# Kernel optimization log

Hardware: AMD Instinct MI355X
Metric: run time of the kernel (lower is better)

Reference implementation:

```python
import jax, jax.numpy as jnp
import numpy as np

DIM = 192
NH = 4
B, H, W = 4, 128, 128


def _conv1x1(x, w, b):
    # x: [b,c,h,w], w: [o,c], b: [o]
    return jnp.einsum('oc,bchw->bohw', w, x) + b[None, :, None, None]


def _dwconv3(x, w, b):
    # depthwise 3x3, w: [C,1,3,3]
    y = jax.lax.conv_general_dilated(
        x, w, window_strides=(1, 1), padding='SAME',
        feature_group_count=x.shape[1],
        dimension_numbers=('NCHW', 'OIHW', 'NCHW'))
    return y + b[None, :, None, None]


def _to_heads(x, nh):
    b, c, h, w = x.shape
    return x.reshape(b, nh, c // nh, h * w)  # b head c (hw)


def _l2norm(x):
    # torch F.normalize(dim=-1): x / max(||x||, eps)
    n = jnp.sqrt(jnp.sum(x * x, axis=-1, keepdims=True))
    return x / jnp.maximum(n, 1e-12)


def _chan_attn(q, k, v, temp):
    # q,k,v: [b,head,c,n]; temp: [head,1,1] -> broadcasts over [b,head,c,c]
    scores = jnp.einsum('bhcn,bhdn->bhcd', q, k) * temp
    a = jax.nn.softmax(scores, axis=-1)
    return jnp.einsum('bhcd,bhdn->bhcn', a, v)


def setup_inputs() -> dict:
    key = jax.random.key(0)
    ks = jax.random.split(key, 16)
    d3 = 3 * DIM
    inp = {
        'sar': jax.random.normal(ks[0], (B, DIM, H, W), jnp.float32),
        'ms': jax.random.normal(ks[1], (B, DIM, H, W), jnp.float32),
        'ms_qkv_w': jax.random.normal(ks[2], (d3, DIM), jnp.float32) * 0.02,
        'ms_qkv_b': jnp.zeros((d3,), jnp.float32),
        'ms_dw_w': jax.random.normal(ks[3], (d3, 1, 3, 3), jnp.float32) * 0.1,
        'ms_dw_b': jnp.zeros((d3,), jnp.float32),
        'ms_temp': jnp.ones((NH, 1, 1), jnp.float32),
        'sar_qkv_w': jax.random.normal(ks[4], (d3, DIM), jnp.float32) * 0.02,
        'sar_qkv_b': jnp.zeros((d3,), jnp.float32),
        'sar_dw_w': jax.random.normal(ks[5], (d3, 1, 3, 3), jnp.float32) * 0.1,
        'sar_dw_b': jnp.zeros((d3,), jnp.float32),
        'sar_temp': jnp.ones((NH, 1, 1), jnp.float32),
        'ms_proj_w': jax.random.normal(ks[6], (DIM, 2 * DIM), jnp.float32) * 0.02,
        'ms_proj_b': jnp.zeros((DIM,), jnp.float32),
        'sar_proj_w': jax.random.normal(ks[7], (DIM, DIM), jnp.float32) * 0.02,
        'sar_proj_b': jnp.zeros((DIM,), jnp.float32),
    }
    return inp


def reference(sar, ms, ms_qkv_w, ms_qkv_b, ms_dw_w, ms_dw_b, ms_temp,
              sar_qkv_w, sar_qkv_b, sar_dw_w, sar_dw_b, sar_temp,
              ms_proj_w, ms_proj_b, sar_proj_w, sar_proj_b):
    b, c, h, w = ms.shape

    ms_qkv = _dwconv3(_conv1x1(ms, ms_qkv_w, ms_qkv_b), ms_dw_w, ms_dw_b)
    ms_q, ms_k, ms_v = jnp.split(ms_qkv, 3, axis=1)
    ms_q = _l2norm(_to_heads(ms_q, NH))
    ms_k = _l2norm(_to_heads(ms_k, NH))
    ms_v = _to_heads(ms_v, NH)

    sar_qkv = _dwconv3(_conv1x1(sar, sar_qkv_w, sar_qkv_b), sar_dw_w, sar_dw_b)
    sar_q, sar_k, sar_v = jnp.split(sar_qkv, 3, axis=1)
    sar_q = _l2norm(_to_heads(sar_q, NH))
    sar_k = _l2norm(_to_heads(sar_k, NH))
    sar_v = _to_heads(sar_v, NH)

    ms_self = _chan_attn(ms_q, ms_k, ms_v, ms_temp).reshape(b, c, h, w)
    sar_self = _chan_attn(sar_q, sar_k, sar_v, sar_temp).reshape(b, c, h, w)
    cross = _chan_attn(sar_q, ms_k, sar_v, ms_temp).reshape(b, c, h, w)

    sar_out = sar + _conv1x1(sar_self, sar_proj_w, sar_proj_b)
    ms_cat = jnp.concatenate([ms_self, cross + ms_self], axis=1)
    ms_out = ms + _conv1x1(ms_cat, ms_proj_w, ms_proj_b)
    return (sar_out, ms_out)
```

## Files before the change

kernel.cpp:

```cpp
#include <hip/hip_runtime.h>
#include <hip/hip_bf16.h>
#include <cstdint>

#define DIMC 192
#define BB 4
#define NN 16384
#define D3 576
#define CHD 48
#define WWID 128
#define HHGT 128
#define NCK 64
#define CKW 256

typedef short short8 __attribute__((ext_vector_type(8)));
typedef float f32x4 __attribute__((ext_vector_type(4)));

union FragU { uint4 u4; short8 s8; };

__device__ __forceinline__ float bf2f(uint16_t v) {
    return __uint_as_float(((uint32_t)v) << 16);
}
__device__ __forceinline__ float2 upk2(uint32_t u) {
    float2 r;
    r.x = __uint_as_float(u << 16);
    r.y = __uint_as_float(u & 0xffff0000u);
    return r;
}
__device__ __forceinline__ uint16_t f2bf(float f) {
    uint32_t x = __float_as_uint(f);
    return (uint16_t)((x + 0x7fffu + ((x >> 16) & 1u)) >> 16);
}
__device__ __forceinline__ uint4 pack8(const uint16_t* v) {
    uint4 u;
    u.x = (uint32_t)v[0] | ((uint32_t)v[1] << 16);
    u.y = (uint32_t)v[2] | ((uint32_t)v[3] << 16);
    u.z = (uint32_t)v[4] | ((uint32_t)v[5] << 16);
    u.w = (uint32_t)v[6] | ((uint32_t)v[7] << 16);
    return u;
}
__device__ __forceinline__ uint4 packf8(float4 lo, float4 hi) {
    uint16_t vv[8] = {f2bf(lo.x), f2bf(lo.y), f2bf(lo.z), f2bf(lo.w),
                      f2bf(hi.x), f2bf(hi.y), f2bf(hi.z), f2bf(hi.w)};
    return pack8(vv);
}

__global__ __launch_bounds__(256, 2) void k_conv_both(
    const float* __restrict__ ms, const float* __restrict__ sarp,
    const float* __restrict__ w_ms, const float* __restrict__ w_sar,
    const float* __restrict__ b_ms, const float* __restrict__ b_sar,
    uint16_t* __restrict__ out_ms, uint16_t* __restrict__ out_sar)
{
    __shared__ uint16_t xs[128][200];
    __shared__ uint16_t wst[64][200];
    const int t = threadIdx.x;
    const int bid = blockIdx.x;
    const int path = bid >> 9;
    const int rem = bid & 511;
    const int nb = rem & 127;
    const int b = rem >> 7;
    const int n0 = nb * 128;

    const float* x      = path ? sarp  : ms;
    const float* wsrc   = path ? w_sar : w_ms;
    const float* bias   = path ? b_sar : b_ms;
    uint16_t* out       = path ? out_sar : out_ms;

    const int lane = t & 63, wvid = t >> 6;
    const int lm = lane & 15, g = lane >> 4;
    const int wm = wvid >> 1, wn = wvid & 1;
    const int wm_ = t >> 2, wq = t & 3;

    {
        const int sn = t & 127, kh = t >> 7;
        const float* xcol = x + ((size_t)b * DIMC + kh * 96) * NN + n0 + sn;
        for (int u = 0; u < 12; ++u) {
            uint16_t vals[8];
#pragma unroll
            for (int j = 0; j < 8; ++j)
                vals[j] = f2bf(xcol[(size_t)(u * 8 + j) * NN]);
            *(uint4*)&xs[sn][(kh * 12 + u) * 8] = pack8(vals);
        }
    }
    {
        const float* wrow = wsrc + (size_t)wm_ * DIMC;
#pragma unroll
        for (int i = 0; i < 6; ++i) {
            const int unit = i * 4 + wq;
            float4 lo = *(const float4*)&wrow[unit * 8];
            float4 hi = *(const float4*)&wrow[unit * 8 + 4];
            *(uint4*)&wst[wm_][unit * 8] = packf8(lo, hi);
        }
    }
    __syncthreads();

    FragU bfr[6][4];
#pragma unroll
    for (int ks = 0; ks < 6; ++ks)
#pragma unroll
        for (int nj = 0; nj < 4; ++nj) {
            const int row = wn * 64 + nj * 16 + lm;
            bfr[ks][nj].u4 = *(const uint4*)&xs[row][ks * 32 + g * 8];
        }
    __syncthreads();

    uint16_t* sw = &xs[0][0] + wvid * (32 * 72);

    for (int mb = 0; mb < 9; ++mb) {
        if (mb) {
            __syncthreads();
            const float* wrow = wsrc + (size_t)(mb * 64 + wm_) * DIMC;
#pragma unroll
            for (int i = 0; i < 6; ++i) {
                const int unit = i * 4 + wq;
                float4 lo = *(const float4*)&wrow[unit * 8];
                float4 hi = *(const float4*)&wrow[unit * 8 + 4];
                *(uint4*)&wst[wm_][unit * 8] = packf8(lo, hi);
            }
            __syncthreads();
        }
        f32x4 acc[2][4];
#pragma unroll
        for (int mi = 0; mi < 2; ++mi)
#pragma unroll
            for (int nj = 0; nj < 4; ++nj) acc[mi][nj] = (f32x4){0.f, 0.f, 0.f, 0.f};
#pragma unroll
        for (int ks = 0; ks < 6; ++ks) {
            FragU afr[2];
#pragma unroll
            for (int mi = 0; mi < 2; ++mi) {
                const int row = wm * 32 + mi * 16 + lm;
                afr[mi].u4 = *(const uint4*)&wst[row][ks * 32 + g * 8];
            }
#pragma unroll
            for (int mi = 0; mi < 2; ++mi)
#pragma unroll
                for (int nj = 0; nj < 4; ++nj)
                    acc[mi][nj] = __builtin_amdgcn_mfma_f32_16x16x32_bf16(
                        afr[mi].s8, bfr[ks][nj].s8, acc[mi][nj], 0, 0, 0);
        }
#pragma unroll
        for (int mi = 0; mi < 2; ++mi) {
            const int rbase = mb * 64 + wm * 32 + mi * 16 + g * 4;
            const float4 bv = *(const float4*)&bias[rbase];
            const float bva[4] = {bv.x, bv.y, bv.z, bv.w};
#pragma unroll
            for (int nj = 0; nj < 4; ++nj)
#pragma unroll
                for (int r = 0; r < 4; ++r)
                    sw[(mi * 16 + g * 4 + r) * 72 + nj * 16 + lm] =
                        f2bf(acc[mi][nj][r] + bva[r]);
        }
        const int l8 = lane & 7, r8 = lane >> 3;
#pragma unroll
        for (int pass = 0; pass < 4; ++pass) {
            const int rr = pass * 8 + r8;
            uint4 v = *(const uint4*)&sw[rr * 72 + l8 * 8];
            const int grow = mb * 64 + wm * 32 + rr;
            *(uint4*)&out[((size_t)b * D3 + grow) * NN + n0 + wn * 64 + l8 * 8] = v;
        }
    }
}

__global__ __launch_bounds__(256, 2) void k_proj_both(
    const uint16_t* __restrict__ sar_self, const uint16_t* __restrict__ ms_self,
    const uint16_t* __restrict__ crossb,
    const float* __restrict__ w_sar, const float* __restrict__ w_ms,
    const float* __restrict__ b_sar, const float* __restrict__ b_ms,
    const float* __restrict__ resid_sar, const float* __restrict__ resid_ms,
    float* __restrict__ out_sar, float* __restrict__ out_ms)
{
    __shared__ uint16_t xs[128][200];
    __shared__ uint16_t wst[64][200];
    const int t = threadIdx.x;
    const int bid = blockIdx.x;
    const int path = bid >> 9;
    const int rem = bid & 511;
    const int nb = rem & 127;
    const int b = rem >> 7;
    const int n0 = nb * 128;
    const int nph = path ? 2 : 1;

    const float* bias  = path ? b_ms : b_sar;
    const float* resid = path ? resid_ms : resid_sar;
    float* out         = path ? out_ms : out_sar;

    const int lane = t & 63, wvid = t >> 6;
    const int lm = lane & 15, g = lane >> 4;
    const int wm = wvid >> 1, wn = wvid & 1;
    const int wm_ = t >> 2, wq = t & 3;

    f32x4 acc[3][2][4];
#pragma unroll
    for (int mb = 0; mb < 3; ++mb)
#pragma unroll
        for (int mi = 0; mi < 2; ++mi)
#pragma unroll
            for (int nj = 0; nj < 4; ++nj) acc[mb][mi][nj] = (f32x4){0.f, 0.f, 0.f, 0.f};

    for (int ph = 0; ph < nph; ++ph) {
        const uint16_t* xsrc = path ? (ph ? crossb : ms_self) : sar_self;
        if (ph) __syncthreads();
        {
            const int sn = t & 127, kh = t >> 7;
            const uint16_t* xcol = xsrc + ((size_t)b * DIMC + kh * 96) * NN + n0 + sn;
            for (int u = 0; u < 12; ++u) {
                uint16_t vals[8];
#pragma unroll
                for (int j = 0; j < 8; ++j)
                    vals[j] = xcol[(size_t)(u * 8 + j) * NN];
                *(uint4*)&xs[sn][(kh * 12 + u) * 8] = pack8(vals);
            }
        }
        {
            const float* wrow = path
                ? w_ms + (size_t)wm_ * 384 + (ph ? 192 : 0)
                : w_sar + (size_t)wm_ * DIMC;
            const bool addb = path && (ph == 0);
#pragma unroll
            for (int i = 0; i < 6; ++i) {
                const int unit = i * 4 + wq;
                float4 lo = *(const float4*)&wrow[unit * 8];
                float4 hi = *(const float4*)&wrow[unit * 8 + 4];
                if (addb) {
                    float4 lo2 = *(const float4*)&wrow[192 + unit * 8];
                    float4 hi2 = *(const float4*)&wrow[192 + unit * 8 + 4];
                    lo.x += lo2.x; lo.y += lo2.y; lo.z += lo2.z; lo.w += lo2.w;
                    hi.x += hi2.x; hi.y += hi2.y; hi.z += hi2.z; hi.w += hi2.w;
                }
                *(uint4*)&wst[wm_][unit * 8] = packf8(lo, hi);
            }
        }
        __syncthreads();
        FragU bfr[6][4];
#pragma unroll
        for (int ks = 0; ks < 6; ++ks)
#pragma unroll
            for (int nj = 0; nj < 4; ++nj) {
                const int row = wn * 64 + nj * 16 + lm;
                bfr[ks][nj].u4 = *(const uint4*)&xs[row][ks * 32 + g * 8];
            }
        for (int mb = 0; mb < 3; ++mb) {
            if (mb) {
                __syncthreads();
                const float* wrow = path
                    ? w_ms + (size_t)(mb * 64 + wm_) * 384 + (ph ? 192 : 0)
                    : w_sar + (size_t)(mb * 64 + wm_) * DIMC;
                const bool addb = path && (ph == 0);
#pragma unroll
                for (int i = 0; i < 6; ++i) {
                    const int unit = i * 4 + wq;
                    float4 lo = *(const float4*)&wrow[unit * 8];
                    float4 hi = *(const float4*)&wrow[unit * 8 + 4];
                    if (addb) {
                        float4 lo2 = *(const float4*)&wrow[192 + unit * 8];
                        float4 hi2 = *(const float4*)&wrow[192 + unit * 8 + 4];
                        lo.x += lo2.x; lo.y += lo2.y; lo.z += lo2.z; lo.w += lo2.w;
                        hi.x += hi2.x; hi.y += hi2.y; hi.z += hi2.z; hi.w += hi2.w;
                    }
                    *(uint4*)&wst[wm_][unit * 8] = packf8(lo, hi);
                }
                __syncthreads();
            }
#pragma unroll
            for (int ks = 0; ks < 6; ++ks) {
                FragU afr[2];
#pragma unroll
                for (int mi = 0; mi < 2; ++mi) {
                    const int row = wm * 32 + mi * 16 + lm;
                    afr[mi].u4 = *(const uint4*)&wst[row][ks * 32 + g * 8];
                }
#pragma unroll
                for (int mi = 0; mi < 2; ++mi)
#pragma unroll
                    for (int nj = 0; nj < 4; ++nj)
                        acc[mb][mi][nj] = __builtin_amdgcn_mfma_f32_16x16x32_bf16(
                            afr[mi].s8, bfr[ks][nj].s8, acc[mb][mi][nj], 0, 0, 0);
            }
        }
    }
#pragma unroll
    for (int mb = 0; mb < 3; ++mb)
#pragma unroll
        for (int mi = 0; mi < 2; ++mi) {
            const int rbase = mb * 64 + wm * 32 + mi * 16 + g * 4;
            const float4 bv = *(const float4*)&bias[rbase];
            const float bva[4] = {bv.x, bv.y, bv.z, bv.w};
#pragma unroll
            for (int nj = 0; nj < 4; ++nj) {
                const int gcol = n0 + wn * 64 + nj * 16 + lm;
#pragma unroll
                for (int r = 0; r < 4; ++r) {
                    const size_t idx = ((size_t)b * DIMC + rbase + r) * NN + gcol;
                    out[idx] = resid[idx] + acc[mb][mi][nj][r] + bva[r];
                }
            }
        }
}

__global__ __launch_bounds__(256) void k_dw_both(
    const uint16_t* __restrict__ in0, const uint16_t* __restrict__ in1,
    const float* __restrict__ w_ms, const float* __restrict__ w_sar,
    const float* __restrict__ b_ms, const float* __restrict__ b_sar,
    uint16_t* __restrict__ out0, uint16_t* __restrict__ out1)
{
    const int t = threadIdx.x;
    int bc = blockIdx.z;
    const int path = (bc >= BB * D3);
    if (path) bc -= BB * D3;
    const int ch = bc % D3;
    const uint16_t* in = path ? in1 : in0;
    const float* w9    = path ? w_sar : w_ms;
    const float* bias  = path ? b_sar : b_ms;
    uint16_t* out      = path ? out1 : out0;

    const int xg = t & 15, yl = t >> 4;
    const int x0 = xg * 8;
    const int y = blockIdx.y * 16 + yl;
    const uint16_t* p = in + (size_t)bc * NN;
    float wv[9];
#pragma unroll
    for (int k = 0; k < 9; ++k) wv[k] = w9[ch * 9 + k];
    float r[3][10];
#pragma unroll
    for (int dy = 0; dy < 3; ++dy) {
        const int yy = y + dy - 1;
        if (yy < 0 || yy >= HHGT) {
#pragma unroll
            for (int j = 0; j < 10; ++j) r[dy][j] = 0.f;
        } else {
            const uint16_t* row = p + yy * WWID;
            uint4 u = *(const uint4*)(row + x0);
            const uint16_t* pv = (const uint16_t*)&u;
#pragma unroll
            for (int j = 0; j < 8; ++j) r[dy][j + 1] = bf2f(pv[j]);
            r[dy][0] = (x0 > 0) ? bf2f(row[x0 - 1]) : 0.f;
            r[dy][9] = (x0 + 8 < WWID) ? bf2f(row[x0 + 8]) : 0.f;
        }
    }
    const float base = bias[ch];
    uint16_t ov[8];
#pragma unroll
    for (int j = 0; j < 8; ++j) {
        float a = base;
#pragma unroll
        for (int dy = 0; dy < 3; ++dy)
#pragma unroll
            for (int dx = 0; dx < 3; ++dx)
                a = fmaf(r[dy][j + dx], wv[dy * 3 + dx], a);
        ov[j] = f2bf(a);
    }
    *(uint4*)(out + (size_t)bc * NN + y * WWID + x0) = pack8(ov);
}

__global__ __launch_bounds__(256) void k_scores_mfma(
    const uint16_t* __restrict__ qkv_ms, const uint16_t* __restrict__ qkv_sar,
    float* __restrict__ partial, float* __restrict__ sumsq)
{
    const int t = threadIdx.x;
    const int bid = blockIdx.x;
    const int ck = bid & (NCK - 1);
    const int pid = bid / NCK;
    const int h = pid & 3, b = pid >> 2;
    const int n0 = ck * CKW;
    const int lane = t & 63, w = t >> 6;

    const uint16_t* qm  = qkv_ms  + ((size_t)b * D3 + h * CHD) * NN;
    const uint16_t* km  = qkv_ms  + ((size_t)b * D3 + DIMC + h * CHD) * NN;
    const uint16_t* qsr = qkv_sar + ((size_t)b * D3 + h * CHD) * NN;
    const uint16_t* ksr = qkv_sar + ((size_t)b * D3 + DIMC + h * CHD) * NN;

    if (w < 3) {
        const uint16_t* qb = (w == 0) ? qm : qsr;
        const uint16_t* kb = (w == 1) ? ksr : km;
        const int lm = lane & 15, g = lane >> 4;
        f32x4 acc[3][3];
#pragma unroll
        for (int i = 0; i < 3; ++i)
#pragma unroll
            for (int j = 0; j < 3; ++j) acc[i][j] = (f32x4){0.f, 0.f, 0.f, 0.f};
#pragma unroll 2
        for (int kk = 0; kk < CKW / 32; ++kk) {
            const int nb2 = n0 + kk * 32 + g * 8;
            FragU qf[3], kf[3];
#pragma unroll
            for (int i = 0; i < 3; ++i)
                qf[i].u4 = *(const uint4*)&qb[(size_t)(i * 16 + lm) * NN + nb2];
#pragma unroll
            for (int j = 0; j < 3; ++j)
                kf[j].u4 = *(const uint4*)&kb[(size_t)(j * 16 + lm) * NN + nb2];
#pragma unroll
            for (int i = 0; i < 3; ++i)
#pragma unroll
                for (int j = 0; j < 3; ++j)
                    acc[i][j] = __builtin_amdgcn_mfma_f32_16x16x32_bf16(
                        qf[i].s8, kf[j].s8, acc[i][j], 0, 0, 0);
        }
        float* pd = partial + (((size_t)pid * 3 + w) * NCK + ck) * 2304;
        const int g4 = g * 4;
#pragma unroll
        for (int i = 0; i < 3; ++i)
#pragma unroll
            for (int j = 0; j < 3; ++j)
#pragma unroll
                for (int r = 0; r < 4; ++r)
                    pd[(i * 16 + g4 + r) * 48 + j * 16 + lm] = acc[i][j][r];
    } else {
#pragma unroll
        for (int rep = 0; rep < 3; ++rep) {
            const int rid = rep * 64 + lane;
            const int s = rid / CHD, c = rid % CHD;
            const uint16_t* rowp =
                (s == 0) ? qm  + (size_t)c * NN :
                (s == 1) ? km  + (size_t)c * NN :
                (s == 2) ? qsr + (size_t)c * NN :
                           ksr + (size_t)c * NN;
            float sum = 0.f;
#pragma unroll 4
            for (int u = 0; u < CKW / 8; ++u) {
                uint4 v = *(const uint4*)&rowp[n0 + u * 8];
                uint32_t uu[4] = {v.x, v.y, v.z, v.w};
#pragma unroll
                for (int q = 0; q < 4; ++q) {
                    float2 f = upk2(uu[q]);
                    sum = fmaf(f.x, f.x, fmaf(f.y, f.y, sum));
                }
            }
            sumsq[(((size_t)pid * NCK + ck) * 4 + s) * CHD + c] = sum;
        }
    }
}

__global__ __launch_bounds__(64) void k_softmax(
    const float* __restrict__ partial, const float* __restrict__ sumsq,
    const float* __restrict__ ms_temp, const float* __restrict__ sar_temp,
    float* __restrict__ A)
{
    const int lane = threadIdx.x;
    const int bi = blockIdx.x;
    const int c = bi % 48;
    const int pid = bi / 48;
    const int h = pid & 3, b = (pid >> 2) & 3, type = pid >> 4;
    const int pid16 = b * 4 + h;
    float s;
    if (lane < 48) {
        float accv = 0.f;
        const float* pp = partial + ((size_t)pid16 * 3 + type) * NCK * 2304 + c * 48 + lane;
#pragma unroll 8
        for (int ck = 0; ck < NCK; ++ck) accv += pp[(size_t)ck * 2304];
        const int qset = (type == 0) ? 0 : 2;
        const int kset = (type == 1) ? 3 : 1;
        float qsum = 0.f, ksum = 0.f;
        const float* sq = sumsq + (size_t)pid16 * NCK * 4 * CHD;
#pragma unroll 8
        for (int ck = 0; ck < NCK; ++ck) {
            qsum += sq[ck * 4 * CHD + qset * CHD + c];
            ksum += sq[ck * 4 * CHD + kset * CHD + lane];
        }
        const float tval = (type == 1) ? sar_temp[h] : ms_temp[h];
        const float qsc = 1.0f / fmaxf(sqrtf(qsum), 1e-12f);
        const float ksc = 1.0f / fmaxf(sqrtf(ksum), 1e-12f);
        s = accv * qsc * ksc * tval;
    } else {
        s = -3.0e38f;
    }
    float m = s;
#pragma unroll
    for (int o = 32; o > 0; o >>= 1) m = fmaxf(m, __shfl_xor(m, o));
    float e = (lane < 48) ? __expf(s - m) : 0.f;
    float sum = e;
#pragma unroll
    for (int o = 32; o > 0; o >>= 1) sum += __shfl_xor(sum, o);
    if (lane < 48) A[(size_t)pid * 2304 + c * 48 + lane] = e / sum;
}

__global__ __launch_bounds__(256) void k_apply_mfma(
    const float* __restrict__ A, const uint16_t* __restrict__ qkv_ms,
    const uint16_t* __restrict__ qkv_sar, uint16_t* __restrict__ attn)
{
    __shared__ uint16_t vs[256][40];
    __shared__ uint16_t as[48][40];
    __shared__ uint16_t sw_all[4][48][72];
    const int t = threadIdx.x;
    const int nb = blockIdx.x & 63;
    const int pid = blockIdx.x >> 6;
    const int h = pid & 3, b = (pid >> 2) & 3, type = pid >> 4;
    const int n0 = nb * 256;
    const uint16_t* vsrc = (type == 0) ? qkv_ms : qkv_sar;
    const uint16_t* vb = vsrc + ((size_t)b * D3 + 2 * DIMC + (size_t)h * CHD) * NN;
    const float* Ap = A + (size_t)pid * 2304;

    const int lane = t & 63, wvid = t >> 6;
    const int lm = lane & 15, g = lane >> 4;

    f32x4 acc[3][4];
#pragma unroll
    for (int i = 0; i < 3; ++i)
#pragma unroll
        for (int j = 0; j < 4; ++j) acc[i][j] = (f32x4){0.f, 0.f, 0.f, 0.f};

    for (int k0 = 0; k0 < 64; k0 += 32) {
        __syncthreads();
#pragma unroll
        for (int kh = 0; kh < 2; ++kh) {
            uint16_t vals[16];
#pragma unroll
            for (int j = 0; j < 16; ++j) {
                const int d = k0 + kh * 16 + j;
                vals[j] = (d < CHD) ? vb[(size_t)d * NN + n0 + t] : (uint16_t)0;
            }
            const int u0 = (2 * kh) ^ ((t >> 3) & 3);
            const int u1 = (2 * kh + 1) ^ ((t >> 3) & 3);
            *(uint4*)&vs[t][u0 * 8] = pack8(&vals[0]);
            *(uint4*)&vs[t][u1 * 8] = pack8(&vals[8]);
        }
        if (t < 192) {
            const int c = t >> 2, dq = t & 3;
            uint16_t av[8];
#pragma unroll
            for (int i = 0; i < 8; ++i) {
                const int d = k0 + dq * 8 + i;
                av[i] = (d < CHD) ? f2bf(Ap[c * CHD + d]) : (uint16_t)0;
            }
            const int u = dq ^ ((c >> 3) & 3);
            *(uint4*)&as[c][u * 8] = pack8(av);
        }
        __syncthreads();
        FragU afr[3], bfr[4];
#pragma unroll
        for (int mi = 0; mi < 3; ++mi) {
            const int row = mi * 16 + lm;
            afr[mi].u4 = *(const uint4*)&as[row][(g ^ ((row >> 3) & 3)) * 8];
        }
#pragma unroll
        for (int nj = 0; nj < 4; ++nj) {
            const int row = wvid * 64 + nj * 16 + lm;
            bfr[nj].u4 = *(const uint4*)&vs[row][(g ^ ((row >> 3) & 3)) * 8];
        }
#pragma unroll
        for (int mi = 0; mi < 3; ++mi)
#pragma unroll
            for (int nj = 0; nj < 4; ++nj)
                acc[mi][nj] = __builtin_amdgcn_mfma_f32_16x16x32_bf16(
                    afr[mi].s8, bfr[nj].s8, acc[mi][nj], 0, 0, 0);
    }

    uint16_t* ob = attn + (size_t)type * BB * DIMC * NN +
                   ((size_t)b * DIMC + (size_t)h * CHD) * NN;
    uint16_t* sw = &sw_all[wvid][0][0];
#pragma unroll
    for (int mi = 0; mi < 3; ++mi)
#pragma unroll
        for (int nj = 0; nj < 4; ++nj)
#pragma unroll
            for (int r = 0; r < 4; ++r)
                sw[(mi * 16 + g * 4 + r) * 72 + nj * 16 + lm] = f2bf(acc[mi][nj][r]);
    const int l8 = lane & 7, r8 = lane >> 3;
#pragma unroll
    for (int pass = 0; pass < 6; ++pass) {
        const int rr = pass * 8 + r8;
        uint4 v = *(const uint4*)&sw[rr * 72 + l8 * 8];
        *(uint4*)&ob[(size_t)rr * NN + n0 + wvid * 64 + l8 * 8] = v;
    }
}

extern "C" void kernel_launch(void* const* d_in, const int* in_sizes, int n_in,
                              void* d_out, int out_size, void* d_ws, size_t ws_size,
                              hipStream_t stream)
{
    const float* sar        = (const float*)d_in[0];
    const float* ms         = (const float*)d_in[1];
    const float* ms_qkv_w   = (const float*)d_in[2];
    const float* ms_qkv_b   = (const float*)d_in[3];
    const float* ms_dw_w    = (const float*)d_in[4];
    const float* ms_dw_b    = (const float*)d_in[5];
    const float* ms_temp    = (const float*)d_in[6];
    const float* sar_qkv_w  = (const float*)d_in[7];
    const float* sar_qkv_b  = (const float*)d_in[8];
    const float* sar_dw_w   = (const float*)d_in[9];
    const float* sar_dw_b   = (const float*)d_in[10];
    const float* sar_temp   = (const float*)d_in[11];
    const float* ms_proj_w  = (const float*)d_in[12];
    const float* ms_proj_b  = (const float*)d_in[13];
    const float* sar_proj_w = (const float*)d_in[14];
    const float* sar_proj_b = (const float*)d_in[15];

    char* ws = (char*)d_ws;
    uint16_t* tmp     = (uint16_t*)(ws);
    uint16_t* tmp2    = (uint16_t*)(d_out);
    uint16_t* qkv_ms  = (uint16_t*)(ws + 75497472ull);
    uint16_t* qkv_sar = (uint16_t*)(ws + 150994944ull);
    float* partial    = (float*)(ws);
    float* sumsq      = (float*)(ws + 33554432ull);
    float* Amat       = (float*)(ws + 230043648ull);
    uint16_t* attn    = tmp;

    float* out_sar = (float*)d_out;
    float* out_ms  = out_sar + (size_t)BB * DIMC * NN;

    dim3 b256(256);
    k_conv_both<<<dim3(1024), b256, 0, stream>>>(
        ms, sar, ms_qkv_w, sar_qkv_w, ms_qkv_b, sar_qkv_b, tmp, tmp2);
    k_dw_both<<<dim3(1, 8, 2 * BB * D3), b256, 0, stream>>>(
        tmp, tmp2, ms_dw_w, sar_dw_w, ms_dw_b, sar_dw_b, qkv_ms, qkv_sar);

    k_scores_mfma<<<dim3(16 * NCK), b256, 0, stream>>>(qkv_ms, qkv_sar, partial, sumsq);
    k_softmax<<<dim3(48 * 48), dim3(64), 0, stream>>>(partial, sumsq, ms_temp, sar_temp, Amat);
    k_apply_mfma<<<dim3(48 * 64), b256, 0, stream>>>(Amat, qkv_ms, qkv_sar, attn);

    uint16_t* ms_self  = attn;
    uint16_t* sar_self = attn + (size_t)BB * DIMC * NN;
    uint16_t* crossb   = attn + 2ull * BB * DIMC * NN;
    k_proj_both<<<dim3(1024), b256, 0, stream>>>(
        sar_self, ms_self, crossb, sar_proj_w, ms_proj_w,
        sar_proj_b, ms_proj_b, sar, ms, out_sar, out_ms);
}
```

Baseline: 347.4 us.

## Pre-convert weights to bf16 and double-buffer weight tiles in GEMM kernels

A new prep kernel converts the qkv and projection weights to bf16 once per call, folding the ms_proj split-sum into a combined weight. The conv and projection kernels then load bf16 weights directly and double-buffer the weight tile in shared memory, prefetching the next tile into registers during the MFMA loop, which removes one barrier per tile. The projection input load is also widened to 32-bit loads that fetch two columns at once. The cost is an extra launch plus register pressure from the prefetch buffers.

```diff
diff --git a/kernel.cpp b/kernel.cpp
--- a/kernel.cpp
+++ b/kernel.cpp
@@ -38,32 +38,48 @@
     u.w = (uint32_t)v[6] | ((uint32_t)v[7] << 16);
     return u;
 }
-__device__ __forceinline__ uint4 packf8(float4 lo, float4 hi) {
-    uint16_t vv[8] = {f2bf(lo.x), f2bf(lo.y), f2bf(lo.z), f2bf(lo.w),
-                      f2bf(hi.x), f2bf(hi.y), f2bf(hi.z), f2bf(hi.w)};
-    return pack8(vv);
+
+__global__ __launch_bounds__(256) void k_prep(
+    const float* __restrict__ w0, const float* __restrict__ w1,
+    const float* __restrict__ w2, const float* __restrict__ w3,
+    uint16_t* __restrict__ o0, uint16_t* __restrict__ o1,
+    uint16_t* __restrict__ o2a, uint16_t* __restrict__ o2b,
+    uint16_t* __restrict__ o3)
+{
+    int i = blockIdx.x * 256 + threadIdx.x;
+    if (i < 110592) { o0[i] = f2bf(w0[i]); return; }
+    i -= 110592;
+    if (i < 110592) { o1[i] = f2bf(w1[i]); return; }
+    i -= 110592;
+    if (i < 36864) {
+        const int o = i / DIMC, c = i % DIMC;
+        o2a[i] = f2bf(w2[o * 384 + c] + w2[o * 384 + DIMC + c]);
+        o2b[i] = f2bf(w2[o * 384 + DIMC + c]);
+        return;
+    }
+    i -= 36864;
+    if (i < 36864) o3[i] = f2bf(w3[i]);
 }
 
 __global__ __launch_bounds__(256, 2) void k_conv_both(
     const float* __restrict__ ms, const float* __restrict__ sarp,
-    const float* __restrict__ w_ms, const float* __restrict__ w_sar,
+    const uint16_t* __restrict__ w_ms, const uint16_t* __restrict__ w_sar,
     const float* __restrict__ b_ms, const float* __restrict__ b_sar,
     uint16_t* __restrict__ out_ms, uint16_t* __restrict__ out_sar)
 {
     __shared__ uint16_t xs[128][200];
-    __shared__ uint16_t wst[64][200];
+    __shared__ uint16_t wstA[64][200];
     const int t = threadIdx.x;
     const int bid = blockIdx.x;
     const int path = bid >> 9;
     const int rem = bid & 511;
-    const int nb = rem & 127;
-    const int b = rem >> 7;
+    const int nb = rem & 127, b = rem >> 7;
     const int n0 = nb * 128;
 
-    const float* x      = path ? sarp  : ms;
-    const float* wsrc   = path ? w_sar : w_ms;
-    const float* bias   = path ? b_sar : b_ms;
-    uint16_t* out       = path ? out_sar : out_ms;
+    const float* x        = path ? sarp  : ms;
+    const uint16_t* wsrc  = path ? w_sar : w_ms;
+    const float* bias     = path ? b_sar : b_ms;
+    uint16_t* out         = path ? out_sar : out_ms;
 
     const int lane = t & 63, wvid = t >> 6;
     const int lm = lane & 15, g = lane >> 4;
@@ -82,13 +98,11 @@
         }
     }
     {
-        const float* wrow = wsrc + (size_t)wm_ * DIMC;
+        const uint16_t* wrow = wsrc + (size_t)wm_ * DIMC;
 #pragma unroll
         for (int i = 0; i < 6; ++i) {
             const int unit = i * 4 + wq;
-            float4 lo = *(const float4*)&wrow[unit * 8];
-            float4 hi = *(const float4*)&wrow[unit * 8 + 4];
-            *(uint4*)&wst[wm_][unit * 8] = packf8(lo, hi);
+            *(uint4*)&wstA[wm_][unit * 8] = *(const uint4*)&wrow[unit * 8];
         }
     }
     __syncthreads();
@@ -103,20 +117,19 @@
         }
     __syncthreads();
 
-    uint16_t* sw = &xs[0][0] + wvid * (32 * 72);
+    uint16_t* xsf  = &xs[0][0];
+    uint16_t* wstB = xsf;
+    uint16_t* sw   = xsf + 12800 + wvid * 2304;
 
     for (int mb = 0; mb < 9; ++mb) {
-        if (mb) {
-            __syncthreads();
-            const float* wrow = wsrc + (size_t)(mb * 64 + wm_) * DIMC;
-#pragma unroll
-            for (int i = 0; i < 6; ++i) {
-                const int unit = i * 4 + wq;
-                float4 lo = *(const float4*)&wrow[unit * 8];
-                float4 hi = *(const float4*)&wrow[unit * 8 + 4];
-                *(uint4*)&wst[wm_][unit * 8] = packf8(lo, hi);
-            }
-            __syncthreads();
+        const uint16_t* cur = (mb & 1) ? wstB : &wstA[0][0];
+        uint16_t* nxt       = (mb & 1) ? &wstA[0][0] : wstB;
+        uint4 wreg[6];
+        if (mb < 8) {
+            const uint16_t* wrow = wsrc + (size_t)((mb + 1) * 64 + wm_) * DIMC;
+#pragma unroll
+            for (int i = 0; i < 6; ++i)
+                wreg[i] = *(const uint4*)&wrow[(i * 4 + wq) * 8];
         }
         f32x4 acc[2][4];
 #pragma unroll
@@ -129,7 +142,7 @@
 #pragma unroll
             for (int mi = 0; mi < 2; ++mi) {
                 const int row = wm * 32 + mi * 16 + lm;
-                afr[mi].u4 = *(const uint4*)&wst[row][ks * 32 + g * 8];
+                afr[mi].u4 = *(const uint4*)&cur[row * 200 + ks * 32 + g * 8];
             }
 #pragma unroll
             for (int mi = 0; mi < 2; ++mi)
@@ -137,6 +150,11 @@
                 for (int nj = 0; nj < 4; ++nj)
                     acc[mi][nj] = __builtin_amdgcn_mfma_f32_16x16x32_bf16(
                         afr[mi].s8, bfr[ks][nj].s8, acc[mi][nj], 0, 0, 0);
+        }
+        if (mb < 8) {
+#pragma unroll
+            for (int i = 0; i < 6; ++i)
+                *(uint4*)&nxt[wm_ * 200 + (i * 4 + wq) * 8] = wreg[i];
         }
 #pragma unroll
         for (int mi = 0; mi < 2; ++mi) {
@@ -158,25 +176,26 @@
             const int grow = mb * 64 + wm * 32 + rr;
             *(uint4*)&out[((size_t)b * D3 + grow) * NN + n0 + wn * 64 + l8 * 8] = v;
         }
+        __syncthreads();
     }
 }
 
 __global__ __launch_bounds__(256, 2) void k_proj_both(
     const uint16_t* __restrict__ sar_self, const uint16_t* __restrict__ ms_self,
     const uint16_t* __restrict__ crossb,
-    const float* __restrict__ w_sar, const float* __restrict__ w_ms,
+    const uint16_t* __restrict__ wp_sar, const uint16_t* __restrict__ wp1_ms,
+    const uint16_t* __restrict__ wp2_ms,
     const float* __restrict__ b_sar, const float* __restrict__ b_ms,
     const float* __restrict__ resid_sar, const float* __restrict__ resid_ms,
     float* __restrict__ out_sar, float* __restrict__ out_ms)
 {
     __shared__ uint16_t xs[128][200];
-    __shared__ uint16_t wst[64][200];
+    __shared__ uint16_t wstA[64][200];
     const int t = threadIdx.x;
     const int bid = blockIdx.x;
     const int path = bid >> 9;
     const int rem = bid & 511;
-    const int nb = rem & 127;
-    const int b = rem >> 7;
+    const int nb = rem & 127, b = rem >> 7;
     const int n0 = nb * 128;
     const int nph = path ? 2 : 1;
 
@@ -189,6 +208,9 @@
     const int wm = wvid >> 1, wn = wvid & 1;
     const int wm_ = t >> 2, wq = t & 3;
 
+    uint16_t* xsf  = &xs[0][0];
+    uint16_t* wstB = xsf;
+
     f32x4 acc[3][2][4];
 #pragma unroll
     for (int mb = 0; mb < 3; ++mb)
@@ -199,35 +221,34 @@
 
     for (int ph = 0; ph < nph; ++ph) {
         const uint16_t* xsrc = path ? (ph ? crossb : ms_self) : sar_self;
-        if (ph) __syncthreads();
+        const uint16_t* wsrc = path ? (ph ? wp2_ms : wp1_ms) : wp_sar;
         {
-            const int sn = t & 127, kh = t >> 7;
-            const uint16_t* xcol = xsrc + ((size_t)b * DIMC + kh * 96) * NN + n0 + sn;
-            for (int u = 0; u < 12; ++u) {
-                uint16_t vals[8];
+            const int p = t & 63, kg = t >> 6;
+            const uint16_t* xcol = xsrc + ((size_t)b * DIMC + kg * 48) * NN + n0 + p * 2;
+            for (int chn = 0; chn < 6; ++chn) {
+                uint32_t v[8];
 #pragma unroll
                 for (int j = 0; j < 8; ++j)
-                    vals[j] = xcol[(size_t)(u * 8 + j) * NN];
-                *(uint4*)&xs[sn][(kh * 12 + u) * 8] = pack8(vals);
+                    v[j] = *(const uint32_t*)&xcol[(size_t)(chn * 8 + j) * NN];
+                uint4 lo4, hi4;
+                lo4.x = (v[0] & 0xffffu) | (v[1] << 16);
+                lo4.y = (v[2] & 0xffffu) | (v[3] << 16);
+                lo4.z = (v[4] & 0xffffu) | (v[5] << 16);
+                lo4.w = (v[6] & 0xffffu) | (v[7] << 16);
+                hi4.x = (v[0] >> 16) | (v[1] & 0xffff0000u);
+                hi4.y = (v[2] >> 16) | (v[3] & 0xffff0000u);
+                hi4.z = (v[4] >> 16) | (v[5] & 0xffff0000u);
+                hi4.w = (v[6] >> 16) | (v[7] & 0xffff0000u);
+                *(uint4*)&xs[p * 2][(kg * 6 + chn) * 8]     = lo4;
+                *(uint4*)&xs[p * 2 + 1][(kg * 6 + chn) * 8] = hi4;
             }
         }
         {
-            const float* wrow = path
-                ? w_ms + (size_t)wm_ * 384 + (ph ? 192 : 0)
-                : w_sar + (size_t)wm_ * DIMC;
-            const bool addb = path && (ph == 0);
+            const uint16_t* wrow = wsrc + (size_t)wm_ * DIMC;
 #pragma unroll
             for (int i = 0; i < 6; ++i) {
                 const int unit = i * 4 + wq;
-                float4 lo = *(const float4*)&wrow[unit * 8];
-                float4 hi = *(const float4*)&wrow[unit * 8 + 4];
-                if (addb) {
-                    float4 lo2 = *(const float4*)&wrow[192 + unit * 8];
-                    float4 hi2 = *(const float4*)&wrow[192 + unit * 8 + 4];
-                    lo.x += lo2.x; lo.y += lo2.y; lo.z += lo2.z; lo.w += lo2.w;
-                    hi.x += hi2.x; hi.y += hi2.y; hi.z += hi2.z; hi.w += hi2.w;
-                }
-                *(uint4*)&wst[wm_][unit * 8] = packf8(lo, hi);
+                *(uint4*)&wstA[wm_][unit * 8] = *(const uint4*)&wrow[unit * 8];
             }
         }
         __syncthreads();
@@ -239,27 +260,17 @@
                 const int row = wn * 64 + nj * 16 + lm;
                 bfr[ks][nj].u4 = *(const uint4*)&xs[row][ks * 32 + g * 8];
             }
+        __syncthreads();
+
         for (int mb = 0; mb < 3; ++mb) {
-            if (mb) {
-                __syncthreads();
-                const float* wrow = path
-                    ? w_ms + (size_t)(mb * 64 + wm_) * 384 + (ph ? 192 : 0)
-                    : w_sar + (size_t)(mb * 64 + wm_) * DIMC;
-                const bool addb = path && (ph == 0);
-#pragma unroll
-                for (int i = 0; i < 6; ++i) {
-                    const int unit = i * 4 + wq;
-                    float4 lo = *(const float4*)&wrow[unit * 8];
-                    float4 hi = *(const float4*)&wrow[unit * 8 + 4];
-                    if (addb) {
-                        float4 lo2 = *(const float4*)&wrow[192 + unit * 8];
-                        float4 hi2 = *(const float4*)&wrow[192 + unit * 8 + 4];
-                        lo.x += lo2.x; lo.y += lo2.y; lo.z += lo2.z; lo.w += lo2.w;
-                        hi.x += hi2.x; hi.y += hi2.y; hi.z += hi2.z; hi.w += hi2.w;
-                    }
-                    *(uint4*)&wst[wm_][unit * 8] = packf8(lo, hi);
-                }
-                __syncthreads();
+            const uint16_t* cur = (mb & 1) ? wstB : &wstA[0][0];
+            uint16_t* nxt       = (mb & 1) ? &wstA[0][0] : wstB;
+            uint4 wreg[6];
+            if (mb < 2) {
+                const uint16_t* wrow = wsrc + (size_t)((mb + 1) * 64 + wm_) * DIMC;
+#pragma unroll
+                for (int i = 0; i < 6; ++i)
+                    wreg[i] = *(const uint4*)&wrow[(i * 4 + wq) * 8];
             }
 #pragma unroll
             for (int ks = 0; ks < 6; ++ks) {
@@ -267,7 +278,7 @@
 #pragma unroll
                 for (int mi = 0; mi < 2; ++mi) {
                     const int row = wm * 32 + mi * 16 + lm;
-                    afr[mi].u4 = *(const uint4*)&wst[row][ks * 32 + g * 8];
+                    afr[mi].u4 = *(const uint4*)&cur[row * 200 + ks * 32 + g * 8];
                 }
 #pragma unroll
                 for (int mi = 0; mi < 2; ++mi)
@@ -276,6 +287,12 @@
                         acc[mb][mi][nj] = __builtin_amdgcn_mfma_f32_16x16x32_bf16(
                             afr[mi].s8, bfr[ks][nj].s8, acc[mb][mi][nj], 0, 0, 0);
             }
+            if (mb < 2) {
+#pragma unroll
+                for (int i = 0; i < 6; ++i)
+                    *(uint4*)&nxt[wm_ * 200 + (i * 4 + wq) * 8] = wreg[i];
+            }
+            __syncthreads();
         }
     }
 #pragma unroll
@@ -592,14 +609,21 @@
     float* partial    = (float*)(ws);
     float* sumsq      = (float*)(ws + 33554432ull);
     float* Amat       = (float*)(ws + 230043648ull);
+    uint16_t* wq_ms   = (uint16_t*)(ws + 230486016ull);
+    uint16_t* wq_sar  = (uint16_t*)(ws + 230707200ull);
+    uint16_t* wp1_ms  = (uint16_t*)(ws + 230928384ull);
+    uint16_t* wp2_ms  = (uint16_t*)(ws + 231002112ull);
+    uint16_t* wp_sar  = (uint16_t*)(ws + 231075840ull);
     uint16_t* attn    = tmp;
 
     float* out_sar = (float*)d_out;
     float* out_ms  = out_sar + (size_t)BB * DIMC * NN;
 
     dim3 b256(256);
+    k_prep<<<dim3(1152), b256, 0, stream>>>(ms_qkv_w, sar_qkv_w, ms_proj_w, sar_proj_w,
+                                            wq_ms, wq_sar, wp1_ms, wp2_ms, wp_sar);
     k_conv_both<<<dim3(1024), b256, 0, stream>>>(
-        ms, sar, ms_qkv_w, sar_qkv_w, ms_qkv_b, sar_qkv_b, tmp, tmp2);
+        ms, sar, wq_ms, wq_sar, ms_qkv_b, sar_qkv_b, tmp, tmp2);
     k_dw_both<<<dim3(1, 8, 2 * BB * D3), b256, 0, stream>>>(
         tmp, tmp2, ms_dw_w, sar_dw_w, ms_dw_b, sar_dw_b, qkv_ms, qkv_sar);
 
@@ -611,6 +635,6 @@
     uint16_t* sar_self = attn + (size_t)BB * DIMC * NN;
     uint16_t* crossb   = attn + 2ull * BB * DIMC * NN;
     k_proj_both<<<dim3(1024), b256, 0, stream>>>(
-        sar_self, ms_self, crossb, sar_proj_w, ms_proj_w,
+        sar_self, ms_self, crossb, wp_sar, wp1_ms, wp2_ms,
         sar_proj_b, ms_proj_b, sar, ms, out_sar, out_ms);
 }
```

New measurement: 307.9 us. 1.13x faster.
